# Kernel optimization log

Measured on AMD Instinct MI355X. Metric: run time of the kernel, lower is better.

## Reference

```python
import jax, jax.numpy as jnp
import numpy as np

INPUT_DIM = 256
N_CLASSES = 100
MAX_DEPTH = 12
N_NODES = 2 ** MAX_DEPTH - 1   # 4095 internal nodes
N_LEAVES = 2 ** MAX_DEPTH      # 4096 leaves


def setup_inputs() -> dict:
    key = jax.random.key(0)
    k_x, k_sf, k_st, k_lp = jax.random.split(key, 4)
    x = jax.random.normal(k_x, (500000, INPUT_DIM), dtype=jnp.float32)
    # split_features ~ U[0, input_dim)  (torch.rand * input_dim)
    split_features = jax.random.uniform(k_sf, (N_NODES,), dtype=jnp.float32) * INPUT_DIM
    split_thresholds = jax.random.normal(k_st, (N_NODES,), dtype=jnp.float32) / np.sqrt(INPUT_DIM)
    # xavier_uniform with gain 1/sqrt(n_classes): bound = gain*sqrt(6/(fan_in+fan_out))
    bound = (1.0 / np.sqrt(N_CLASSES)) * np.sqrt(6.0 / (N_LEAVES + N_CLASSES))
    leaf_probabilities = jax.random.uniform(
        k_lp, (N_LEAVES, N_CLASSES), dtype=jnp.float32, minval=-bound, maxval=bound)
    return {"x": x, "split_features": split_features,
            "split_thresholds": split_thresholds,
            "leaf_probabilities": leaf_probabilities}


def reference(x, split_features, split_thresholds, leaf_probabilities):
    batch = x.shape[0]
    # per-node feature index: floor then clamp to [0, input_dim-1]
    node_features = jnp.clip(jnp.floor(split_features), 0, INPUT_DIM - 1).astype(jnp.int32)
    node_idx = jnp.zeros((batch,), dtype=jnp.int32)
    for _ in range(MAX_DEPTH):  # fixed small unrolled traversal
        feats = node_features[node_idx]                       # [B]
        thr = split_thresholds[node_idx]                      # [B]
        vals = jnp.take_along_axis(x, feats[:, None], axis=1)[:, 0]  # [B]
        node_idx = node_idx * 2 + 1 + (vals > thr).astype(jnp.int32)
    leaf_idx = node_idx - N_NODES                             # [B] in [0, N_LEAVES)
    return jax.nn.softmax(leaf_probabilities[leaf_idx], axis=1)
```

## Files before the change

kernel.cpp:

```cpp
#include <hip/hip_runtime.h>
#include <math.h>

#define INPUT_DIM 256
#define N_CLASSES 100
#define MAX_DEPTH 12
#define N_NODES   4095
#define N_LEAVES  4096

#define TPB   512
#define NWAVE 8
#define RPW   5
#define DEPTH 3
#define ROWP  260
#define NF4   (N_CLASSES / 4)
#define NBLK  256

#define WAITV(N) asm volatile("s_waitcnt vmcnt(" #N ")" ::: "memory")
#define SCHEDB() __builtin_amdgcn_sched_barrier(0)

typedef float f32x4 __attribute__((ext_vector_type(4)));

__device__ __forceinline__ void async_load16(const void* gsrc, void* ldst) {
    __builtin_amdgcn_global_load_lds(
        (const __attribute__((address_space(1))) unsigned int*)gsrc,
        (__attribute__((address_space(3))) unsigned int*)ldst, 16, 0, 0);
}

__global__ __launch_bounds__(64) void softmax_rows_kernel(
    const float* __restrict__ lp, float* __restrict__ tab) {
    const int row  = blockIdx.x;
    const int lane = threadIdx.x;
    const float* src = lp + (size_t)row * N_CLASSES;

    float v0 = src[lane];
    float v1 = (lane + 64 < N_CLASSES) ? src[lane + 64] : -INFINITY;

    float m = fmaxf(v0, v1);
    #pragma unroll
    for (int off = 32; off > 0; off >>= 1) m = fmaxf(m, __shfl_xor(m, off));

    float e0 = expf(v0 - m);
    float e1 = (lane + 64 < N_CLASSES) ? expf(v1 - m) : 0.0f;
    float s = e0 + e1;
    #pragma unroll
    for (int off = 32; off > 0; off >>= 1) s += __shfl_xor(s, off);

    const float inv = 1.0f / s;
    tab[(size_t)row * N_CLASSES + lane] = e0 * inv;
    if (lane + 64 < N_CLASSES)
        tab[(size_t)row * N_CLASSES + lane + 64] = e1 * inv;
}

__global__ __launch_bounds__(TPB) void traverse_kernel(
    const float* __restrict__ x,
    const float* __restrict__ split_features,
    const float* __restrict__ split_thresholds,
    unsigned short* __restrict__ leaf_out,
    int batch, int nunits) {
    __shared__ float         s_rows[NWAVE][DEPTH][RPW][ROWP];
    __shared__ float         s_thr[N_NODES];
    __shared__ unsigned char s_feat[N_NODES + 1];

    const int tid  = threadIdx.x;
    const int wid  = tid >> 6;
    const int lane = tid & 63;

    for (int i = tid; i < N_NODES; i += TPB) {
        s_thr[i] = split_thresholds[i];
        int f = (int)floorf(split_features[i]);
        s_feat[i] = (unsigned char)min(max(f, 0), INPUT_DIM - 1);
    }
    __syncthreads();

    const int NPIPE = gridDim.x * NWAVE;
    const int W     = blockIdx.x * NWAVE + wid;

    auto stage = [&](int k, int slot) {
        long g = (long)W + (long)k * NPIPE;
        if (g >= nunits) g = nunits - 1;
        #pragma unroll
        for (int j = 0; j < RPW; ++j) {
            long r = g * RPW + j;
            if (r >= batch) r = batch - 1;
            const float* src = x + (size_t)r * INPUT_DIM + lane * 4;
            async_load16((const void*)src, (void*)&s_rows[wid][slot][j][0]);
        }
    };

    stage(0, 0);
    stage(1, 1);

    for (int k = 0; ; ++k) {
        const long g = (long)W + (long)k * NPIPE;
        if (g >= nunits) break;

        stage(k + 2, (k + 2) % 3);
        SCHEDB();
        if (k == 0)      WAITV(10);
        else if (k == 1) WAITV(11);
        else             WAITV(12);
        SCHEDB();

        if (lane < RPW) {
            const float* row = &s_rows[wid][k % 3][lane][0];
            float t = s_thr[0];
            int   f = s_feat[0];
            int   n = 0;
            #pragma unroll
            for (int d = 0; d < MAX_DEPTH; ++d) {
                const int l = 2 * n + 1;
                if (d < MAX_DEPTH - 1) {
                    const float tl = s_thr[l],  tr = s_thr[l + 1];
                    const int   fl = s_feat[l], fr = s_feat[l + 1];
                    const int go = row[f] > t ? 1 : 0;
                    t = go ? tr : tl;
                    f = go ? fr : fl;
                    n = l + go;
                } else {
                    n = l + (row[f] > t ? 1 : 0);
                }
            }
            const long s = g * RPW + lane;
            if (s < batch)
                leaf_out[s] = (unsigned short)(n - N_NODES);
        }
    }
}

__global__ __launch_bounds__(256) void gather_out_kernel(
    const f32x4* __restrict__ tab4,
    const unsigned short* __restrict__ leaf,
    f32x4* __restrict__ out4, int total4) {
    for (int j = blockIdx.x * 256 + threadIdx.x; j < total4;
         j += gridDim.x * 256) {
        const int r = j / NF4;
        const int q = j - r * NF4;
        const int lf = leaf[r];
        f32x4 v = tab4[(size_t)lf * NF4 + q];
        __builtin_nontemporal_store(v, &out4[j]);
    }
}

__global__ __launch_bounds__(256) void fused_kernel(
    const float* __restrict__ x,
    const float* __restrict__ split_features,
    const float* __restrict__ split_thresholds,
    const float* __restrict__ lp,
    float* __restrict__ out, int batch) {
    __shared__ float2 s_nodes[N_NODES];
    for (int i = threadIdx.x; i < N_NODES; i += blockDim.x) {
        int f = (int)floorf(split_features[i]);
        f = min(max(f, 0), INPUT_DIM - 1);
        float2 n; n.x = split_thresholds[i]; n.y = __int_as_float(f);
        s_nodes[i] = n;
    }
    __syncthreads();

    const int b = blockIdx.x * blockDim.x + threadIdx.x;
    if (b >= batch) return;

    const float* row = x + (size_t)b * INPUT_DIM;
    int node = 0;
    #pragma unroll
    for (int d = 0; d < MAX_DEPTH; ++d) {
        const float2 n = s_nodes[node];
        const float val = row[__float_as_int(n.y)];
        node = 2 * node + 1 + (val > n.x ? 1 : 0);
    }
    const int leaf = node - N_NODES;

    const float* src = lp + (size_t)leaf * N_CLASSES;
    float m = -INFINITY;
    for (int cidx = 0; cidx < N_CLASSES; ++cidx) m = fmaxf(m, src[cidx]);
    float s = 0.0f;
    float e[N_CLASSES];
    for (int cidx = 0; cidx < N_CLASSES; ++cidx) { e[cidx] = expf(src[cidx] - m); s += e[cidx]; }
    const float inv = 1.0f / s;
    float* dst = out + (size_t)b * N_CLASSES;
    for (int cidx = 0; cidx < N_CLASSES; ++cidx) dst[cidx] = e[cidx] * inv;
}

extern "C" void kernel_launch(void* const* d_in, const int* in_sizes, int n_in,
                              void* d_out, int out_size, void* d_ws, size_t ws_size,
                              hipStream_t stream) {
    const float* x  = (const float*)d_in[0];
    const float* sf = (const float*)d_in[1];
    const float* st = (const float*)d_in[2];
    const float* lp = (const float*)d_in[3];
    float* out = (float*)d_out;

    const int batch = in_sizes[0] / INPUT_DIM;

    const size_t tab_bytes = (size_t)N_LEAVES * N_CLASSES * sizeof(float);
    const size_t need = tab_bytes + (size_t)batch * sizeof(unsigned short);

    if (ws_size >= need && batch > 0) {
        float* tab = (float*)d_ws;
        unsigned short* leaf = (unsigned short*)((char*)d_ws + tab_bytes);

        softmax_rows_kernel<<<N_LEAVES, 64, 0, stream>>>(lp, tab);

        const int nunits = (batch + RPW - 1) / RPW;
        int nblk = (nunits + NWAVE - 1) / NWAVE;
        if (nblk > NBLK) nblk = NBLK;
        traverse_kernel<<<nblk, TPB, 0, stream>>>(
            x, sf, st, leaf, batch, nunits);

        const int total4 = batch * NF4;
        int nb2 = (total4 + 255) / 256;
        if (nb2 > 2048) nb2 = 2048;
        gather_out_kernel<<<nb2, 256, 0, stream>>>(
            (const f32x4*)tab, leaf, (f32x4*)out, total4);
    } else {
        fused_kernel<<<(batch + 255) / 256, 256, 0, stream>>>(
            x, sf, st, lp, out, batch);
    }
}
```

Baseline: 140.2 us.

## Pipeline tree traversal and output gather across batch segments in one kernel

Merges the traversal and gather kernels into a single kernel whose blocks are split into traversal blocks and gather blocks. It is launched five times over four batch segments, so gathering segment t-1 runs at the same time as traversing segment t. The per-wave row pipeline drops from triple to double buffering with 3 rows per wave instead of 5. The goal is to overlap the read-bound traversal with the write-bound output gather, at the cost of extra launches and re-initialising the node table in every step.

```diff
diff --git a/kernel.cpp b/kernel.cpp
--- a/kernel.cpp
+++ b/kernel.cpp
@@ -7,13 +7,17 @@
 #define N_NODES   4095
 #define N_LEAVES  4096
 
-#define TPB   512
-#define NWAVE 8
-#define RPW   5
-#define DEPTH 3
-#define ROWP  260
-#define NF4   (N_CLASSES / 4)
-#define NBLK  256
+#define S_SEG  4
+#define TBLK   256
+#define GBLK   256
+#define NBLK   (TBLK + GBLK)
+#define TPB    512
+#define NWAVE  8
+#define NPIPES (TBLK * NWAVE)
+#define RPW    3
+#define TBUF   2
+#define ROWP   260
+#define NF4    (N_CLASSES / 4)
 
 #define WAITV(N) asm volatile("s_waitcnt vmcnt(" #N ")" ::: "memory")
 #define SCHEDB() __builtin_amdgcn_sched_barrier(0)
@@ -51,13 +55,17 @@
         tab[(size_t)row * N_CLASSES + lane + 64] = e1 * inv;
 }
 
-__global__ __launch_bounds__(TPB) void traverse_kernel(
+__global__ __launch_bounds__(TPB) void tree_step_kernel(
     const float* __restrict__ x,
     const float* __restrict__ split_features,
     const float* __restrict__ split_thresholds,
-    unsigned short* __restrict__ leaf_out,
-    int batch, int nunits) {
-    __shared__ float         s_rows[NWAVE][DEPTH][RPW][ROWP];
+    const f32x4* __restrict__ tab4,
+    unsigned short* __restrict__ leaf,
+    f32x4* __restrict__ out4,
+    int batch,
+    int u0, int u1,
+    int j40, int j41) {
+    __shared__ float         s_rows[NWAVE][TBUF][RPW][ROWP];
     __shared__ float         s_thr[N_NODES];
     __shared__ unsigned char s_feat[N_NODES + 1];
 
@@ -65,79 +73,76 @@
     const int wid  = tid >> 6;
     const int lane = tid & 63;
 
-    for (int i = tid; i < N_NODES; i += TPB) {
-        s_thr[i] = split_thresholds[i];
-        int f = (int)floorf(split_features[i]);
-        s_feat[i] = (unsigned char)min(max(f, 0), INPUT_DIM - 1);
-    }
-    __syncthreads();
-
-    const int NPIPE = gridDim.x * NWAVE;
-    const int W     = blockIdx.x * NWAVE + wid;
-
-    auto stage = [&](int k, int slot) {
-        long g = (long)W + (long)k * NPIPE;
-        if (g >= nunits) g = nunits - 1;
-        #pragma unroll
-        for (int j = 0; j < RPW; ++j) {
-            long r = g * RPW + j;
-            if (r >= batch) r = batch - 1;
-            const float* src = x + (size_t)r * INPUT_DIM + lane * 4;
-            async_load16((const void*)src, (void*)&s_rows[wid][slot][j][0]);
-        }
-    };
-
-    stage(0, 0);
-    stage(1, 1);
-
-    for (int k = 0; ; ++k) {
-        const long g = (long)W + (long)k * NPIPE;
-        if (g >= nunits) break;
-
-        stage(k + 2, (k + 2) % 3);
-        SCHEDB();
-        if (k == 0)      WAITV(10);
-        else if (k == 1) WAITV(11);
-        else             WAITV(12);
-        SCHEDB();
-
-        if (lane < RPW) {
-            const float* row = &s_rows[wid][k % 3][lane][0];
-            float t = s_thr[0];
-            int   f = s_feat[0];
-            int   n = 0;
+    if (blockIdx.x < TBLK) {
+        for (int i = tid; i < N_NODES; i += TPB) {
+            s_thr[i] = split_thresholds[i];
+            int f = (int)floorf(split_features[i]);
+            s_feat[i] = (unsigned char)min(max(f, 0), INPUT_DIM - 1);
+        }
+        __syncthreads();
+
+        const int span = u1 - u0;
+        const int pipe = blockIdx.x * NWAVE + wid;
+        const int nk = (pipe < span) ? ((span - 1 - pipe) / NPIPES + 1) : 0;
+
+        auto stage = [&](int k, int slot) {
+            const long g = (long)u0 + pipe + (long)k * NPIPES;
             #pragma unroll
-            for (int d = 0; d < MAX_DEPTH; ++d) {
-                const int l = 2 * n + 1;
-                if (d < MAX_DEPTH - 1) {
-                    const float tl = s_thr[l],  tr = s_thr[l + 1];
-                    const int   fl = s_feat[l], fr = s_feat[l + 1];
-                    const int go = row[f] > t ? 1 : 0;
-                    t = go ? tr : tl;
-                    f = go ? fr : fl;
-                    n = l + go;
-                } else {
-                    n = l + (row[f] > t ? 1 : 0);
+            for (int j = 0; j < RPW; ++j) {
+                long r = g * RPW + j;
+                if (r >= batch) r = batch - 1;
+                const float* src = x + (size_t)r * INPUT_DIM + lane * 4;
+                async_load16((const void*)src, (void*)&s_rows[wid][slot][j][0]);
+            }
+        };
+
+        if (nk > 0) stage(0, 0);
+
+        for (int k = 0; k < nk; ++k) {
+            const bool more = (k + 1 < nk);
+            if (more) stage(k + 1, (k + 1) & 1);
+            SCHEDB();
+            if (k == 0) { if (more) WAITV(3); else WAITV(0); }
+            else       { if (more) WAITV(4); else WAITV(1); }
+            SCHEDB();
+
+            int leafv = 0;
+            if (lane < RPW) {
+                const float* row = &s_rows[wid][k & 1][lane][0];
+                float t = s_thr[0];
+                int   f = s_feat[0];
+                int   n = 0;
+                #pragma unroll
+                for (int d = 0; d < MAX_DEPTH; ++d) {
+                    const int l = 2 * n + 1;
+                    if (d < MAX_DEPTH - 1) {
+                        const float tl = s_thr[l],  tr = s_thr[l + 1];
+                        const int   fl = s_feat[l], fr = s_feat[l + 1];
+                        const int go = row[f] > t ? 1 : 0;
+                        t = go ? tr : tl;
+                        f = go ? fr : fl;
+                        n = l + go;
+                    } else {
+                        n = l + (row[f] > t ? 1 : 0);
+                    }
                 }
+                leafv = n - N_NODES;
             }
-            const long s = g * RPW + lane;
-            if (s < batch)
-                leaf_out[s] = (unsigned short)(n - N_NODES);
-        }
-    }
-}
-
-__global__ __launch_bounds__(256) void gather_out_kernel(
-    const f32x4* __restrict__ tab4,
-    const unsigned short* __restrict__ leaf,
-    f32x4* __restrict__ out4, int total4) {
-    for (int j = blockIdx.x * 256 + threadIdx.x; j < total4;
-         j += gridDim.x * 256) {
-        const int r = j / NF4;
-        const int q = j - r * NF4;
-        const int lf = leaf[r];
-        f32x4 v = tab4[(size_t)lf * NF4 + q];
-        __builtin_nontemporal_store(v, &out4[j]);
+
+            const long rowbase = ((long)u0 + pipe + (long)k * NPIPES) * RPW;
+            if (lane < RPW && rowbase + lane < batch)
+                leaf[rowbase + lane] = (unsigned short)leafv;
+        }
+        WAITV(0);
+    } else {
+        const int gid = blockIdx.x - TBLK;
+        for (int j = j40 + gid * TPB + tid; j < j41; j += GBLK * TPB) {
+            const int r  = j / NF4;
+            const int q  = j - r * NF4;
+            const int lf = leaf[r];
+            f32x4 v = tab4[(size_t)lf * NF4 + q];
+            __builtin_nontemporal_store(v, &out4[j]);
+        }
     }
 }
 
@@ -171,13 +176,13 @@
 
     const float* src = lp + (size_t)leaf * N_CLASSES;
     float m = -INFINITY;
-    for (int cidx = 0; cidx < N_CLASSES; ++cidx) m = fmaxf(m, src[cidx]);
+    for (int c = 0; c < N_CLASSES; ++c) m = fmaxf(m, src[c]);
     float s = 0.0f;
     float e[N_CLASSES];
-    for (int cidx = 0; cidx < N_CLASSES; ++cidx) { e[cidx] = expf(src[cidx] - m); s += e[cidx]; }
+    for (int c = 0; c < N_CLASSES; ++c) { e[c] = expf(src[c] - m); s += e[c]; }
     const float inv = 1.0f / s;
     float* dst = out + (size_t)b * N_CLASSES;
-    for (int cidx = 0; cidx < N_CLASSES; ++cidx) dst[cidx] = e[cidx] * inv;
+    for (int c = 0; c < N_CLASSES; ++c) dst[c] = e[c] * inv;
 }
 
 extern "C" void kernel_launch(void* const* d_in, const int* in_sizes, int n_in,
@@ -191,26 +196,35 @@
 
     const int batch = in_sizes[0] / INPUT_DIM;
 
-    const size_t tab_bytes = (size_t)N_LEAVES * N_CLASSES * sizeof(float);
-    const size_t need = tab_bytes + (size_t)batch * sizeof(unsigned short);
-
-    if (ws_size >= need && batch > 0) {
-        float* tab = (float*)d_ws;
+    const size_t tab_bytes  = (size_t)N_LEAVES * N_CLASSES * sizeof(float);
+    const size_t leaf_bytes = (size_t)batch * sizeof(unsigned short);
+    const size_t need = tab_bytes + leaf_bytes;
+
+    if (ws_size >= need && batch >= 4096) {
+        float*          tab  = (float*)d_ws;
         unsigned short* leaf = (unsigned short*)((char*)d_ws + tab_bytes);
 
         softmax_rows_kernel<<<N_LEAVES, 64, 0, stream>>>(lp, tab);
 
         const int nunits = (batch + RPW - 1) / RPW;
-        int nblk = (nunits + NWAVE - 1) / NWAVE;
-        if (nblk > NBLK) nblk = NBLK;
-        traverse_kernel<<<nblk, TPB, 0, stream>>>(
-            x, sf, st, leaf, batch, nunits);
-
-        const int total4 = batch * NF4;
-        int nb2 = (total4 + 255) / 256;
-        if (nb2 > 2048) nb2 = 2048;
-        gather_out_kernel<<<nb2, 256, 0, stream>>>(
-            (const f32x4*)tab, leaf, (f32x4*)out, total4);
+
+        int ub[S_SEG + 1], j4b[S_SEG + 1];
+        for (int i = 0; i <= S_SEG; ++i) {
+            ub[i] = (int)((long)nunits * i / S_SEG);
+            long rb = (long)ub[i] * RPW;
+            if (rb > batch) rb = batch;
+            j4b[i] = (int)(rb * NF4);
+        }
+
+        for (int t = 0; t <= S_SEG; ++t) {
+            const int tu0 = (t < S_SEG) ? ub[t]     : 0;
+            const int tu1 = (t < S_SEG) ? ub[t + 1] : 0;
+            const int gj0 = (t > 0)     ? j4b[t - 1] : 0;
+            const int gj1 = (t > 0)     ? j4b[t]     : 0;
+            tree_step_kernel<<<NBLK, TPB, 0, stream>>>(
+                x, sf, st, (const f32x4*)tab, leaf, (f32x4*)out,
+                batch, tu0, tu1, gj0, gj1);
+        }
     } else {
         fused_kernel<<<(batch + 255) / 256, 256, 0, stream>>>(
             x, sf, st, lp, out, batch);
```

New measurement: 169.7 us. +21.0%, slower.

## Rework traversal pipeline to double-buffered prefetch with more blocks and fewer rows per wave

Applied to the files above, without the earlier changes.

The traversal kernel moves from a triple-buffered, 5-rows-per-wave prefetch over 256 blocks to a double-buffered, 3-rows-per-wave scheme over 512 blocks. Each wave now computes its exact iteration count, so it no longer issues clamped dummy loads past the end. The goal is more waves in flight across the GPU to hide latency on the mostly-random row gathers, with less LDS per block. In exchange, each wave keeps only one load stage in flight ahead of compute, which gives less latency hiding per wave.

```diff
diff --git a/kernel.cpp b/kernel.cpp
--- a/kernel.cpp
+++ b/kernel.cpp
@@ -7,13 +7,14 @@
 #define N_NODES   4095
 #define N_LEAVES  4096
 
-#define TPB   512
-#define NWAVE 8
-#define RPW   5
-#define DEPTH 3
-#define ROWP  260
-#define NF4   (N_CLASSES / 4)
-#define NBLK  256
+#define TPB    512
+#define NWAVE  8
+#define TBLK   512
+#define NPIPES (TBLK * NWAVE)
+#define RPW    3
+#define TBUF   2
+#define ROWP   260
+#define NF4    (N_CLASSES / 4)
 
 #define WAITV(N) asm volatile("s_waitcnt vmcnt(" #N ")" ::: "memory")
 #define SCHEDB() __builtin_amdgcn_sched_barrier(0)
@@ -57,7 +58,7 @@
     const float* __restrict__ split_thresholds,
     unsigned short* __restrict__ leaf_out,
     int batch, int nunits) {
-    __shared__ float         s_rows[NWAVE][DEPTH][RPW][ROWP];
+    __shared__ float         s_rows[NWAVE][TBUF][RPW][ROWP];
     __shared__ float         s_thr[N_NODES];
     __shared__ unsigned char s_feat[N_NODES + 1];
 
@@ -72,12 +73,11 @@
     }
     __syncthreads();
 
-    const int NPIPE = gridDim.x * NWAVE;
-    const int W     = blockIdx.x * NWAVE + wid;
+    const int pipe = blockIdx.x * NWAVE + wid;
+    const int nk = (pipe < nunits) ? ((nunits - 1 - pipe) / NPIPES + 1) : 0;
 
     auto stage = [&](int k, int slot) {
-        long g = (long)W + (long)k * NPIPE;
-        if (g >= nunits) g = nunits - 1;
+        const long g = (long)pipe + (long)k * NPIPES;
         #pragma unroll
         for (int j = 0; j < RPW; ++j) {
             long r = g * RPW + j;
@@ -87,22 +87,19 @@
         }
     };
 
-    stage(0, 0);
-    stage(1, 1);
-
-    for (int k = 0; ; ++k) {
-        const long g = (long)W + (long)k * NPIPE;
-        if (g >= nunits) break;
-
-        stage(k + 2, (k + 2) % 3);
+    if (nk > 0) stage(0, 0);
+
+    for (int k = 0; k < nk; ++k) {
+        const bool more = (k + 1 < nk);
+        if (more) stage(k + 1, (k + 1) & 1);
         SCHEDB();
-        if (k == 0)      WAITV(10);
-        else if (k == 1) WAITV(11);
-        else             WAITV(12);
+        if (k == 0) { if (more) WAITV(3); else WAITV(0); }
+        else        { if (more) WAITV(4); else WAITV(1); }
         SCHEDB();
 
+        int leafv = 0;
         if (lane < RPW) {
-            const float* row = &s_rows[wid][k % 3][lane][0];
+            const float* row = &s_rows[wid][k & 1][lane][0];
             float t = s_thr[0];
             int   f = s_feat[0];
             int   n = 0;
@@ -120,11 +117,14 @@
                     n = l + (row[f] > t ? 1 : 0);
                 }
             }
-            const long s = g * RPW + lane;
-            if (s < batch)
-                leaf_out[s] = (unsigned short)(n - N_NODES);
+            leafv = n - N_NODES;
         }
-    }
+
+        const long rowbase = ((long)pipe + (long)k * NPIPES) * RPW;
+        if (lane < RPW && rowbase + lane < batch)
+            leaf_out[rowbase + lane] = (unsigned short)leafv;
+    }
+    WAITV(0);
 }
 
 __global__ __launch_bounds__(256) void gather_out_kernel(
@@ -171,13 +171,13 @@
 
     const float* src = lp + (size_t)leaf * N_CLASSES;
     float m = -INFINITY;
-    for (int cidx = 0; cidx < N_CLASSES; ++cidx) m = fmaxf(m, src[cidx]);
+    for (int c = 0; c < N_CLASSES; ++c) m = fmaxf(m, src[c]);
     float s = 0.0f;
     float e[N_CLASSES];
-    for (int cidx = 0; cidx < N_CLASSES; ++cidx) { e[cidx] = expf(src[cidx] - m); s += e[cidx]; }
+    for (int c = 0; c < N_CLASSES; ++c) { e[c] = expf(src[c] - m); s += e[c]; }
     const float inv = 1.0f / s;
     float* dst = out + (size_t)b * N_CLASSES;
-    for (int cidx = 0; cidx < N_CLASSES; ++cidx) dst[cidx] = e[cidx] * inv;
+    for (int c = 0; c < N_CLASSES; ++c) dst[c] = e[c] * inv;
 }
 
 extern "C" void kernel_launch(void* const* d_in, const int* in_sizes, int n_in,
@@ -194,7 +194,7 @@
     const size_t tab_bytes = (size_t)N_LEAVES * N_CLASSES * sizeof(float);
     const size_t need = tab_bytes + (size_t)batch * sizeof(unsigned short);
 
-    if (ws_size >= need && batch > 0) {
+    if (ws_size >= need && batch >= 4096) {
         float* tab = (float*)d_ws;
         unsigned short* leaf = (unsigned short*)((char*)d_ws + tab_bytes);
 
@@ -202,7 +202,7 @@
 
         const int nunits = (batch + RPW - 1) / RPW;
         int nblk = (nunits + NWAVE - 1) / NWAVE;
-        if (nblk > NBLK) nblk = NBLK;
+        if (nblk > TBLK) nblk = TBLK;
         traverse_kernel<<<nblk, TPB, 0, stream>>>(
             x, sf, st, leaf, batch, nunits);
 
```

Result: no change. 138.9 us (-1.0%).
